# Kernel optimization log

Measured on AMD Instinct MI355X. Metric: run time of the kernel, lower is better.

## Reference

```python
import jax, jax.numpy as jnp
import numpy as np

EPS = 1e-12  # matches torch F.normalize eps

def _l2norm(v, axis):
    n = jnp.sqrt(jnp.sum(v * v, axis=axis, keepdims=True))
    return v / jnp.maximum(n, EPS)

def setup_inputs() -> dict:
    key = jax.random.key(0)
    k1, k2, k3 = jax.random.split(key, 3)
    N, D, H, W, K = 64, 128, 60, 80, 64
    x = jax.random.normal(k1, (N, D, H, W), dtype=jnp.float32)
    conv_w = jax.random.normal(k2, (K, D), dtype=jnp.float32) * 0.1
    centroids = jax.random.uniform(k3, (K, D), dtype=jnp.float32)
    return {"x": x, "conv_w": conv_w, "centroids": centroids}

def reference(x, conv_w, centroids):
    N, D, H, W = x.shape
    K = conv_w.shape[0]
    # descriptor-wise L2 normalization over channel dim
    x = _l2norm(x, axis=1)
    xf = x.reshape(N, D, H * W)                       # [N, D, P]
    # 1x1 conv (no bias) == matmul over channels, then softmax over clusters
    logits = jnp.einsum('kd,ndp->nkp', conv_w, xf)    # [N, K, P]
    sa = jax.nn.softmax(logits, axis=1)               # [N, K, P]
    # vlad[n,k,:] = sum_p sa[n,k,p] * (xf[n,:,p] - centroids[k])
    agg = jnp.einsum('nkp,ndp->nkd', sa, xf)          # [N, K, D]
    vlad = agg - sa.sum(axis=-1)[..., None] * centroids[None]
    vlad = _l2norm(vlad, axis=2)                      # intra-normalization
    vlad = vlad.reshape(N, K * D)
    vlad = _l2norm(vlad, axis=1)                      # global L2 norm
    return vlad
```

## Files before the change

### kernel.cpp

```cpp
#include <hip/hip_runtime.h>
#include <hip/hip_bf16.h>
#include <hip/hip_fp16.h>
#include <math.h>

#define NN 64
#define DD 128
#define PP 4800
#define KK 64
#define BPN 15
#define PB  320
#define CP  64
#define NCH 5

#define WT  136
#define XPT 136
#define XDT 72
#define SAT 72

#define PAGG_SZ  ((size_t)NN * BPN * KK * DD)
#define PSSUM_SZ ((size_t)NN * BPN * KK)

typedef __attribute__((ext_vector_type(8))) short bf16x8;
typedef __attribute__((ext_vector_type(4))) float f32x4;

__device__ __forceinline__ unsigned short f2bf(float f) {
  unsigned u = __float_as_uint(f);
  u += 0x7fffu + ((u >> 16) & 1u);
  return (unsigned short)(u >> 16);
}
__device__ __forceinline__ unsigned pk2(float a, float b) {
  union { __hip_bfloat162 h2; unsigned u; } cv;
  cv.h2 = __float22bfloat162_rn(make_float2(a, b));
  return cv.u;
}

__global__ __launch_bounds__(256, 2) void main_kernel(const float* __restrict__ x,
                                                      const float* __restrict__ conv_w,
                                                      __half* __restrict__ pagg,
                                                      float* __restrict__ pssum) {
  __shared__ __align__(16) unsigned short w_s[KK * WT];
  __shared__ __align__(16) unsigned short xpd[CP * XPT];
  __shared__ __align__(16) unsigned short xdp[DD * XDT];
  __shared__ __align__(16) unsigned short sa_s[KK * SAT];
  __shared__ float red_s[256];

  const int b = blockIdx.x;
  const int n = b / BPN, sl = b % BPN;
  const int t = threadIdx.x, lane = t & 63, wv = t >> 6;
  const int lq = lane >> 4, ll = lane & 15;
  const int pb = t & 7, db = t >> 3;

  {
    int k = t >> 2, h = t & 3;
    const float* wp = conv_w + k * DD + h * 32;
    unsigned short* dst = &w_s[k * WT + h * 32];
#pragma unroll
    for (int i = 0; i < 4; ++i) {
      float4 a = *(const float4*)(wp + 8 * i);
      float4 c = *(const float4*)(wp + 8 * i + 4);
      uint4 o = {pk2(a.x, a.y), pk2(a.z, a.w), pk2(c.x, c.y), pk2(c.z, c.w)};
      *(uint4*)&dst[8 * i] = o;
    }
  }
  if (t < 64) red_s[t] = 0.f;

  const float* xb = x + (size_t)n * DD * PP + (size_t)(4 * db) * PP + sl * PB + 8 * pb;

  float4 pf[8];
#pragma unroll
  for (int r = 0; r < 4; ++r) {
    pf[2 * r]     = *(const float4*)(xb + (size_t)r * PP);
    pf[2 * r + 1] = *(const float4*)(xb + (size_t)r * PP + 4);
  }

  f32x4 acc[8];
#pragma unroll
  for (int i = 0; i < 8; ++i) acc[i] = (f32x4){0.f, 0.f, 0.f, 0.f};
  float ssacc[16];
#pragma unroll
  for (int i = 0; i < 16; ++i) ssacc[i] = 0.f;

  for (int c = 0; c < NCH; ++c) {
    float4 cur[8];
#pragma unroll
    for (int i = 0; i < 8; ++i) cur[i] = pf[i];
    if (c + 1 < NCH) {
      const float* xc = xb + (c + 1) * CP;
#pragma unroll
      for (int r = 0; r < 4; ++r) {
        pf[2 * r]     = *(const float4*)(xc + (size_t)r * PP);
        pf[2 * r + 1] = *(const float4*)(xc + (size_t)r * PP + 4);
      }
    }

    float sq[8];
#pragma unroll
    for (int h = 0; h < 2; ++h)
#pragma unroll
      for (int j = 0; j < 4; ++j) {
        float s = 0.f;
#pragma unroll
        for (int r = 0; r < 4; ++r) {
          float v = (&cur[2 * r + h].x)[j];
          s = fmaf(v, v, s);
        }
        sq[4 * h + j] = s;
      }
#pragma unroll
    for (int i = 0; i < 8; ++i) {
      sq[i] += __shfl_xor(sq[i], 8);
      sq[i] += __shfl_xor(sq[i], 16);
      sq[i] += __shfl_xor(sq[i], 32);
    }

    __syncthreads();

    if (lane < 8) {
#pragma unroll
      for (int j = 0; j < 8; ++j) atomicAdd(&red_s[8 * lane + j], sq[j]);
    }

    {
      unsigned prow[4][4];
#pragma unroll
      for (int r = 0; r < 4; ++r) {
        const float4& a = cur[2 * r];
        const float4& c2 = cur[2 * r + 1];
        prow[r][0] = pk2(a.x, a.y);
        prow[r][1] = pk2(a.z, a.w);
        prow[r][2] = pk2(c2.x, c2.y);
        prow[r][3] = pk2(c2.z, c2.w);
        uint4 o = {prow[r][0], prow[r][1], prow[r][2], prow[r][3]};
        *(uint4*)&xdp[(4 * db + r) * XDT + 8 * pb] = o;
      }
      const int colh = (((db >> 1) ^ pb) << 3) + (db & 1) * 4;
#pragma unroll
      for (int j2 = 0; j2 < 4; ++j2) {
        unsigned lo01 = __builtin_amdgcn_perm(prow[1][j2], prow[0][j2], 0x05040100u);
        unsigned hi01 = __builtin_amdgcn_perm(prow[1][j2], prow[0][j2], 0x07060302u);
        unsigned lo23 = __builtin_amdgcn_perm(prow[3][j2], prow[2][j2], 0x05040100u);
        unsigned hi23 = __builtin_amdgcn_perm(prow[3][j2], prow[2][j2], 0x07060302u);
        int p_e = 8 * pb + 2 * j2;
        *(uint2*)&xpd[p_e * XPT + colh]       = make_uint2(lo01, lo23);
        *(uint2*)&xpd[(p_e + 1) * XPT + colh] = make_uint2(hi01, hi23);
      }
    }
    __syncthreads();

    {
      const int prow_ = wv * 16 + ll;
      const int swz = (2 * wv + (ll >> 3)) & 7;
      f32x4 lg[4];
#pragma unroll
      for (int kt = 0; kt < 4; ++kt) lg[kt] = (f32x4){0.f, 0.f, 0.f, 0.f};
#pragma unroll
      for (int ks = 0; ks < 4; ++ks) {
        bf16x8 bfrag = *(const bf16x8*)&xpd[prow_ * XPT + ((((ks << 2) | lq) ^ swz) << 3)];
#pragma unroll
        for (int kt = 0; kt < 4; ++kt) {
          bf16x8 afrag = *(const bf16x8*)&w_s[(kt * 16 + ll) * WT + ks * 32 + lq * 8];
          lg[kt] = __builtin_amdgcn_mfma_f32_16x16x32_bf16(afrag, bfrag, lg[kt], 0, 0, 0);
        }
      }
      float iv = 1.0f / fmaxf(sqrtf(red_s[prow_]), 1e-12f);
      float vals[16];
      float m = -1e30f;
#pragma unroll
      for (int kt = 0; kt < 4; ++kt)
#pragma unroll
        for (int r = 0; r < 4; ++r) {
          float v = lg[kt][r] * iv;
          vals[kt * 4 + r] = v;
          m = fmaxf(m, v);
        }
      m = fmaxf(m, __shfl_xor(m, 16));
      m = fmaxf(m, __shfl_xor(m, 32));
      float se = 0.f;
#pragma unroll
      for (int i = 0; i < 16; ++i) {
        float e = __expf(vals[i] - m);
        vals[i] = e;
        se += e;
      }
      se += __shfl_xor(se, 16);
      se += __shfl_xor(se, 32);
      float rinv = 1.0f / se;
      float r2 = rinv * iv;
#pragma unroll
      for (int kt = 0; kt < 4; ++kt)
#pragma unroll
        for (int r = 0; r < 4; ++r) {
          float e = vals[kt * 4 + r];
          ssacc[kt * 4 + r] += e * rinv;
          sa_s[(kt * 16 + lq * 4 + r) * SAT + prow_] = f2bf(e * r2);
        }
    }
    __syncthreads();
    if (c + 1 < NCH && t < 64) red_s[t] = 0.f;

#pragma unroll
    for (int ks = 0; ks < 2; ++ks) {
      bf16x8 afrag = *(const bf16x8*)&sa_s[(wv * 16 + ll) * SAT + ks * 32 + lq * 8];
#pragma unroll
      for (int dt = 0; dt < 8; ++dt) {
        bf16x8 bfrag = *(const bf16x8*)&xdp[(dt * 16 + ll) * XDT + ks * 32 + lq * 8];
        acc[dt] = __builtin_amdgcn_mfma_f32_16x16x32_bf16(afrag, bfrag, acc[dt], 0, 0, 0);
      }
    }
  }

  {
    __half* base = pagg + (size_t)(n * BPN + sl) * (KK * DD);
#pragma unroll
    for (int dt = 0; dt < 8; ++dt)
#pragma unroll
      for (int r = 0; r < 4; ++r)
        base[(16 * wv + 4 * lq + r) * DD + dt * 16 + ll] = __float2half(acc[dt][r]);
  }
#pragma unroll
  for (int i = 0; i < 16; ++i) {
    float s = ssacc[i];
    s += __shfl_xor(s, 1);
    s += __shfl_xor(s, 2);
    s += __shfl_xor(s, 4);
    s += __shfl_xor(s, 8);
    if (ll == 0) red_s[wv * 64 + (i >> 2) * 16 + lq * 4 + (i & 3)] = s;
  }
  __syncthreads();
  if (t < 64)
    pssum[(n * BPN + sl) * KK + t] =
        red_s[t] + red_s[64 + t] + red_s[128 + t] + red_s[192 + t];
}

__global__ __launch_bounds__(256) void ep_kernel(const __half* __restrict__ pagg,
                                                 const float* __restrict__ pssum,
                                                 const float* __restrict__ cent,
                                                 float* __restrict__ out) {
  const int blk = blockIdx.x;
  const int n = blk >> 3, kg = blk & 7;
  const int t = threadIdx.x;
  const int kl = t >> 5, c32 = t & 31;
  const int k = kg * 8 + kl;
  const size_t off = (size_t)k * DD + c32 * 4;

  const __half* base = pagg + (size_t)n * BPN * (KK * DD) + off;
  float4 a = {0.f, 0.f, 0.f, 0.f};
  for (int s = 0; s < BPN; ++s) {
    uint2 u = *(const uint2*)(base + (size_t)s * (KK * DD));
    __half2 h0 = *(const __half2*)&u.x;
    __half2 h1 = *(const __half2*)&u.y;
    float2 f0 = __half22float2(h0);
    float2 f1 = __half22float2(h1);
    a.x += f0.x; a.y += f0.y; a.z += f1.x; a.w += f1.y;
  }
  float sk = 0.f;
  for (int s = 0; s < BPN; ++s) sk += pssum[(n * BPN + s) * KK + k];

  float4 c4 = *(const float4*)(cent + off);
  float4 v;
  v.x = fmaf(-sk, c4.x, a.x);
  v.y = fmaf(-sk, c4.y, a.y);
  v.z = fmaf(-sk, c4.z, a.z);
  v.w = fmaf(-sk, c4.w, a.w);

  float ss = v.x * v.x + v.y * v.y + v.z * v.z + v.w * v.w;
  ss += __shfl_xor(ss, 1);
  ss += __shfl_xor(ss, 2);
  ss += __shfl_xor(ss, 4);
  ss += __shfl_xor(ss, 8);
  ss += __shfl_xor(ss, 16);
  float scale = 0.125f / fmaxf(sqrtf(ss), 1e-12f);
  v.x *= scale; v.y *= scale; v.z *= scale; v.w *= scale;
  *(float4*)(out + (size_t)n * (KK * DD) + off) = v;
}

extern "C" void kernel_launch(void* const* d_in, const int* in_sizes, int n_in,
                              void* d_out, int out_size, void* d_ws, size_t ws_size,
                              hipStream_t stream) {
  const float* x      = (const float*)d_in[0];
  const float* conv_w = (const float*)d_in[1];
  const float* cent   = (const float*)d_in[2];
  float* out = (float*)d_out;
  float* ws  = (float*)d_ws;

  __half* pagg = (__half*)ws;
  float* pssum = ws + PAGG_SZ / 2;

  main_kernel<<<NN * BPN, 256, 0, stream>>>(x, conv_w, pagg, pssum);
  ep_kernel<<<NN * 8, 256, 0, stream>>>(pagg, pssum, cent, out);
}
```

Measured before the change: 241.2 us.

## Use ds_read_b64_tr_b16 transpose loads instead of a second transposed LDS copy

```diff
diff --git a/kernel.cpp b/kernel.cpp
--- a/kernel.cpp
+++ b/kernel.cpp
@@ -13,15 +13,16 @@
 #define NCH 5
 
 #define WT  136
-#define XPT 136
-#define XDT 72
 #define SAT 72
+#define TSTR 72
 
 #define PAGG_SZ  ((size_t)NN * BPN * KK * DD)
 #define PSSUM_SZ ((size_t)NN * BPN * KK)
 
 typedef __attribute__((ext_vector_type(8))) short bf16x8;
 typedef __attribute__((ext_vector_type(4))) float f32x4;
+typedef __attribute__((ext_vector_type(2))) unsigned int u32x2;
+typedef __attribute__((address_space(3))) const unsigned short lds_cus;
 
 __device__ __forceinline__ unsigned short f2bf(float f) {
   unsigned u = __float_as_uint(f);
@@ -34,13 +35,16 @@
   return cv.u;
 }
 
-__global__ __launch_bounds__(256, 2) void main_kernel(const float* __restrict__ x,
+#define TR_READ(dst, addr, imm)                                          \
+  asm volatile("ds_read_b64_tr_b16 %0, %1 offset:" #imm                  \
+               : "=v"(dst) : "v"(addr))
+
+__global__ __launch_bounds__(256, 3) void main_kernel(const float* __restrict__ x,
                                                       const float* __restrict__ conv_w,
                                                       __half* __restrict__ pagg,
                                                       float* __restrict__ pssum) {
   __shared__ __align__(16) unsigned short w_s[KK * WT];
-  __shared__ __align__(16) unsigned short xpd[CP * XPT];
-  __shared__ __align__(16) unsigned short xdp[DD * XDT];
+  __shared__ __align__(16) unsigned short xdp[128 * TSTR];
   __shared__ __align__(16) unsigned short sa_s[KK * SAT];
   __shared__ float red_s[256];
 
@@ -80,6 +84,11 @@
 #pragma unroll
   for (int i = 0; i < 16; ++i) ssacc[i] = 0.f;
 
+  const int wbase = (db * 4 + (pb >> 1)) * TSTR + 8 * (pb & 1);
+  const unsigned trbase =
+      (unsigned)(size_t)((lds_cus*)xdp + (8 * lq + wv) * TSTR + 4 * ll);
+  const int g2base = ((ll >> 2) * 4 + (lq >> 1)) * TSTR + (ll & 3) * 16 + (lq & 1) * 8;
+
   for (int c = 0; c < NCH; ++c) {
     float4 cur[8];
 #pragma unroll
@@ -121,41 +130,41 @@
     }
 
     {
-      unsigned prow[4][4];
 #pragma unroll
       for (int r = 0; r < 4; ++r) {
         const float4& a = cur[2 * r];
         const float4& c2 = cur[2 * r + 1];
-        prow[r][0] = pk2(a.x, a.y);
-        prow[r][1] = pk2(a.z, a.w);
-        prow[r][2] = pk2(c2.x, c2.y);
-        prow[r][3] = pk2(c2.z, c2.w);
-        uint4 o = {prow[r][0], prow[r][1], prow[r][2], prow[r][3]};
-        *(uint4*)&xdp[(4 * db + r) * XDT + 8 * pb] = o;
-      }
-      const int colh = (((db >> 1) ^ pb) << 3) + (db & 1) * 4;
-#pragma unroll
-      for (int j2 = 0; j2 < 4; ++j2) {
-        unsigned lo01 = __builtin_amdgcn_perm(prow[1][j2], prow[0][j2], 0x05040100u);
-        unsigned hi01 = __builtin_amdgcn_perm(prow[1][j2], prow[0][j2], 0x07060302u);
-        unsigned lo23 = __builtin_amdgcn_perm(prow[3][j2], prow[2][j2], 0x05040100u);
-        unsigned hi23 = __builtin_amdgcn_perm(prow[3][j2], prow[2][j2], 0x07060302u);
-        int p_e = 8 * pb + 2 * j2;
-        *(uint2*)&xpd[p_e * XPT + colh]       = make_uint2(lo01, lo23);
-        *(uint2*)&xpd[(p_e + 1) * XPT + colh] = make_uint2(hi01, hi23);
+        uint4 o = {pk2(a.x, a.y), pk2(a.z, a.w), pk2(c2.x, c2.y), pk2(c2.z, c2.w)};
+        *(uint4*)&xdp[wbase + r * 16] = o;
       }
     }
     __syncthreads();
 
     {
       const int prow_ = wv * 16 + ll;
-      const int swz = (2 * wv + (ll >> 3)) & 7;
+      u32x2 trv[8];
+      TR_READ(trv[0], trbase, 0);
+      TR_READ(trv[1], trbase, 576);
+      TR_READ(trv[2], trbase, 4608);
+      TR_READ(trv[3], trbase, 5184);
+      TR_READ(trv[4], trbase, 9216);
+      TR_READ(trv[5], trbase, 9792);
+      TR_READ(trv[6], trbase, 13824);
+      TR_READ(trv[7], trbase, 14400);
+      asm volatile("s_waitcnt lgkmcnt(0)" ::: "memory");
+      __builtin_amdgcn_sched_barrier(0);
+
       f32x4 lg[4];
 #pragma unroll
       for (int kt = 0; kt < 4; ++kt) lg[kt] = (f32x4){0.f, 0.f, 0.f, 0.f};
 #pragma unroll
       for (int ks = 0; ks < 4; ++ks) {
-        bf16x8 bfrag = *(const bf16x8*)&xpd[prow_ * XPT + ((((ks << 2) | lq) ^ swz) << 3)];
+        union { unsigned u[4]; bf16x8 v; } bu;
+        bu.u[0] = trv[2 * ks].x;
+        bu.u[1] = trv[2 * ks].y;
+        bu.u[2] = trv[2 * ks + 1].x;
+        bu.u[3] = trv[2 * ks + 1].y;
+        bf16x8 bfrag = bu.v;
 #pragma unroll
         for (int kt = 0; kt < 4; ++kt) {
           bf16x8 afrag = *(const bf16x8*)&w_s[(kt * 16 + ll) * WT + ks * 32 + lq * 8];
@@ -203,7 +212,7 @@
       bf16x8 afrag = *(const bf16x8*)&sa_s[(wv * 16 + ll) * SAT + ks * 32 + lq * 8];
 #pragma unroll
       for (int dt = 0; dt < 8; ++dt) {
-        bf16x8 bfrag = *(const bf16x8*)&xdp[(dt * 16 + ll) * XDT + ks * 32 + lq * 8];
+        bf16x8 bfrag = *(const bf16x8*)&xdp[g2base + dt * (16 * TSTR) + ks * (2 * TSTR)];
         acc[dt] = __builtin_amdgcn_mfma_f32_16x16x32_bf16(afrag, bfrag, acc[dt], 0, 0, 0);
       }
     }
```

Result: no change. 238.8 us (-1.0%).
